# Performance work log

Measured on AMD Instinct MI355X. Metric: run time of the kernel, lower is better.

The kernel has to match this reference:

```python
import jax, jax.numpy as jnp
import numpy as np

TOP_K = 2


def setup_inputs() -> dict:
    key = jax.random.key(0)
    ks = jax.random.split(key, 5)
    B, S, D, F, E = 2, 1024, 1024, 4096, 8
    return {
        "hidden_states": jax.random.normal(ks[0], (B, S, D), jnp.float32),
        "gate_w": jax.random.normal(ks[1], (E, D), jnp.float32) * 0.02,
        "w1": jax.random.normal(ks[2], (E, D, F), jnp.float32) * 0.02,
        "w2": jax.random.normal(ks[3], (E, F, D), jnp.float32) * 0.02,
        "w3": jax.random.normal(ks[4], (E, D, F), jnp.float32) * 0.02,
    }


def reference(hidden_states, gate_w, w1, w2, w3):
    B, S, D = hidden_states.shape
    E = gate_w.shape[0]
    x = hidden_states.reshape(-1, D).astype(jnp.float32)  # [T, D]
    T = x.shape[0]

    # Router: softmax over experts, top-k, renormalize selected weights.
    router_logits = x @ gate_w.T                      # [T, E]
    probs = jax.nn.softmax(router_logits, axis=-1)
    top_w, top_e = jax.lax.top_k(probs, TOP_K)        # [T, K]
    top_w = top_w / jnp.sum(top_w, axis=-1, keepdims=True)

    # Combine weights [T, E]: weight of expert e for token t (0 if not selected).
    combine = jnp.zeros((T, E), jnp.float32).at[jnp.arange(T)[:, None], top_e].add(top_w)

    # Expert SwiGLU FFNs (vectorized over experts; unselected contributions are
    # zeroed by combine weights, matching the gather/scatter math exactly).
    h = jnp.einsum('td,edf->etf', x, w1)              # [E, T, F]
    g = jnp.einsum('td,edf->etf', x, w3)              # [E, T, F]
    y = jnp.einsum('etf,efd->etd', jax.nn.silu(h) * g, w2)  # [E, T, D]

    out = jnp.einsum('etd,te->td', y, combine)        # weighted scatter-combine
    return out.reshape(B, S, D), router_logits
```

## Files before the change

### kernel.cpp

```cpp
#include <hip/hip_runtime.h>
#include <hip/hip_bf16.h>
#include <math.h>

#define T_TOK   2048
#define DDIM    1024
#define FDIM    4096
#define NEXP    8
#define MAXROWS 4608

typedef __bf16          bf16x8 __attribute__((ext_vector_type(8)));
typedef float           f32x4  __attribute__((ext_vector_type(4)));
typedef unsigned short  u16x8  __attribute__((ext_vector_type(8)));

#define LDSP 40
#define FCW  128

static __device__ __forceinline__ unsigned short f2b(float f) {
    __hip_bfloat16 h = __float2bfloat16(f);
    return __builtin_bit_cast(unsigned short, h);
}

static __device__ __forceinline__ void gll16(const unsigned short* g, unsigned short* l) {
    __builtin_amdgcn_global_load_lds(
        (const __attribute__((address_space(1))) unsigned int*)g,
        (__attribute__((address_space(3))) unsigned int*)l, 16, 0, 0);
}

__global__ __launch_bounds__(256) void moe_router_kernel(
    const float* __restrict__ x, const float* __restrict__ gate_w,
    float* __restrict__ logits_out, int* __restrict__ top_e, float* __restrict__ top_w)
{
    int wid  = (blockIdx.x * blockDim.x + threadIdx.x) >> 6;
    int lane = threadIdx.x & 63;
    if (wid >= T_TOK) return;
    const float* xr = x + (size_t)wid * DDIM;
    float acc[NEXP];
    #pragma unroll
    for (int e = 0; e < NEXP; ++e) acc[e] = 0.f;
    for (int d = lane; d < DDIM; d += 64) {
        float xv = xr[d];
        #pragma unroll
        for (int e = 0; e < NEXP; ++e) acc[e] += xv * gate_w[e * DDIM + d];
    }
    #pragma unroll
    for (int e = 0; e < NEXP; ++e) {
        #pragma unroll
        for (int off = 32; off > 0; off >>= 1)
            acc[e] += __shfl_down(acc[e], off, 64);
    }
    if (lane == 0) {
        #pragma unroll
        for (int e = 0; e < NEXP; ++e) logits_out[wid * NEXP + e] = acc[e];
        int e1 = 0;
        #pragma unroll
        for (int e = 1; e < NEXP; ++e) if (acc[e] > acc[e1]) e1 = e;
        int e2 = (e1 == 0) ? 1 : 0;
        #pragma unroll
        for (int e = 0; e < NEXP; ++e) if (e != e1 && acc[e] > acc[e2]) e2 = e;
        float p2 = __expf(acc[e2] - acc[e1]);
        float s  = 1.0f + p2;
        top_e[wid * 2]     = e1;
        top_e[wid * 2 + 1] = e2;
        top_w[wid * 2]     = 1.0f / s;
        top_w[wid * 2 + 1] = p2 / s;
    }
}

__global__ void moe_scatter_kernel(const int* __restrict__ top_e, const float* __restrict__ top_w,
                                   int* __restrict__ cnt, int* __restrict__ list_tok,
                                   float* __restrict__ list_w)
{
    int t = blockIdx.x * blockDim.x + threadIdx.x;
    if (t >= T_TOK) return;
    #pragma unroll
    for (int s = 0; s < 2; ++s) {
        int e   = top_e[t * 2 + s];
        int pos = atomicAdd(&cnt[e], 1);
        list_tok[e * T_TOK + pos] = t;
        list_w [e * T_TOK + pos] = top_w[t * 2 + s];
    }
}

__global__ void moe_prefix_kernel(const int* __restrict__ cnt, int* __restrict__ offs)
{
    if (threadIdx.x == 0 && blockIdx.x == 0) {
        int o = 0;
        #pragma unroll
        for (int e = 0; e < NEXP; ++e) { offs[e] = o; o += ((cnt[e] + 63) >> 6) << 6; }
        offs[NEXP] = o;
    }
}

__global__ __launch_bounds__(256) void transpose_cvt_kernel(
    const float* __restrict__ src, unsigned short* __restrict__ dst, int R, int C)
{
    int tilesC = C >> 6;
    int tilesPerMat = (R >> 6) * tilesC;
    int e  = blockIdx.x / tilesPerMat;
    int t  = blockIdx.x - e * tilesPerMat;
    int tr = t / tilesC, tc = t - tr * tilesC;
    const float*    s = src + (size_t)e * R * C + (size_t)(tr * 64) * C + tc * 64;
    unsigned short* d = dst + (size_t)e * R * C + (size_t)(tc * 64) * R + tr * 64;

    __shared__ unsigned short lds[64][72];
    int tid = threadIdx.x;
    int rr = tid >> 4, cc = (tid & 15) * 4;
    #pragma unroll
    for (int i = 0; i < 4; ++i) {
        int r = rr + 16 * i;
        float4 v = *(const float4*)(s + (size_t)r * C + cc);
        lds[cc + 0][r] = f2b(v.x); lds[cc + 1][r] = f2b(v.y);
        lds[cc + 2][r] = f2b(v.z); lds[cc + 3][r] = f2b(v.w);
    }
    __syncthreads();
    int orow = tid >> 2, oc = (tid & 3) * 16;
    u16x8 a = *(const u16x8*)&lds[orow][oc];
    u16x8 b = *(const u16x8*)&lds[orow][oc + 8];
    *(u16x8*)(d + (size_t)orow * R + oc)     = a;
    *(u16x8*)(d + (size_t)orow * R + oc + 8) = b;
}

__global__ __launch_bounds__(256) void moe_gather_kernel(
    const float* __restrict__ x, const int* __restrict__ list_tok,
    const int* __restrict__ cnt, const int* __restrict__ offs,
    unsigned short* __restrict__ xg)
{
    int e  = blockIdx.x >> 8;
    int rb = blockIdx.x & 255;
    int n = cnt[e];
    int npad = (n + 63) & ~63;
    if (rb * 8 >= npad) return;
    int base = offs[e];
    int tid = threadIdx.x;
    #pragma unroll
    for (int i = 0; i < 4; ++i) {
        int u = tid + 256 * i;
        int r = u >> 7, cu = u & 127;
        int slot = rb * 8 + r;
        int tok = list_tok[e * T_TOK + slot];
        const float* sp = x + (size_t)tok * DDIM + cu * 8;
        float4 v0 = *(const float4*)(sp);
        float4 v1 = *(const float4*)(sp + 4);
        u16x8 t8;
        t8[0]=f2b(v0.x); t8[1]=f2b(v0.y); t8[2]=f2b(v0.z); t8[3]=f2b(v0.w);
        t8[4]=f2b(v1.x); t8[5]=f2b(v1.y); t8[6]=f2b(v1.z); t8[7]=f2b(v1.w);
        *(u16x8*)(xg + (size_t)(base + slot) * DDIM + cu * 8) = t8;
    }
}

__global__ __launch_bounds__(256, 2) void moe_up_kernel(
    const unsigned short* __restrict__ xg,
    const unsigned short* __restrict__ w1t, const unsigned short* __restrict__ w3t,
    const int* __restrict__ cnt, const int* __restrict__ offs,
    unsigned short* __restrict__ act)
{
    const int NWG = NEXP * 32 * 16;
    int logical = (blockIdx.x & 7) * (NWG >> 3) + (blockIdx.x >> 3);
    int mt = logical & 15;
    int fc = (logical >> 4) & 31;
    int e  = logical >> 9;
    int n = cnt[e];
    int npad = (n + 63) & ~63;
    if (mt * 128 >= npad) return;
    int rowBase  = offs[e] + mt * 128;
    int rowMax   = offs[e] + npad - 1;
    int rowLimit = offs[e] + npad;

    __shared__ unsigned short As [128 * 32];
    __shared__ unsigned short B1s[128 * 32];
    __shared__ unsigned short B2s[128 * 32];

    int tid = threadIdx.x;
    int lane = tid & 63, wv = tid >> 6;
    int c = lane & 15, g = lane >> 4;
    int wr = (wv >> 1) * 64, wc = (wv & 1) * 64;

    int srow = tid >> 2, skc = tid & 3;
    int r0 = min(rowBase + srow,      rowMax);
    int r1 = min(rowBase + 64 + srow, rowMax);
    const unsigned short* gA0 = xg + (size_t)r0 * DDIM + skc * 8;
    const unsigned short* gA1 = xg + (size_t)r1 * DDIM + skc * 8;
    size_t wb = (size_t)e * FDIM * DDIM + (size_t)(fc * 128 + srow) * DDIM + skc * 8;
    const unsigned short* gB1a = w1t + wb;
    const unsigned short* gB1b = w1t + wb + (size_t)64 * DDIM;
    const unsigned short* gB2a = w3t + wb;
    const unsigned short* gB2b = w3t + wb + (size_t)64 * DDIM;
    unsigned short* lA0 = As  + tid * 8;
    unsigned short* lA1 = As  + 2048 + tid * 8;
    unsigned short* lB1a = B1s + tid * 8;
    unsigned short* lB1b = B1s + 2048 + tid * 8;
    unsigned short* lB2a = B2s + tid * 8;
    unsigned short* lB2b = B2s + 2048 + tid * 8;

    f32x4 acc_h[4][4], acc_g[4][4];
    #pragma unroll
    for (int i = 0; i < 4; ++i)
        #pragma unroll
        for (int j = 0; j < 4; ++j) { acc_h[i][j] = (f32x4)(0.f); acc_g[i][j] = (f32x4)(0.f); }

    for (int k0 = 0; k0 < DDIM; k0 += 32) {
        gll16(gA0  + k0, lA0);
        gll16(gA1  + k0, lA1);
        gll16(gB1a + k0, lB1a);
        gll16(gB1b + k0, lB1b);
        gll16(gB2a + k0, lB2a);
        gll16(gB2b + k0, lB2b);
        __syncthreads();

        bf16x8 af[4];
        #pragma unroll
        for (int mi = 0; mi < 4; ++mi)
            af[mi] = *reinterpret_cast<const bf16x8*>(&As[(wr + mi * 16 + c) * 32 + g * 8]);
        #pragma unroll
        for (int ni = 0; ni < 4; ++ni) {
            bf16x8 b1 = *reinterpret_cast<const bf16x8*>(&B1s[(wc + ni * 16 + c) * 32 + g * 8]);
            bf16x8 b2 = *reinterpret_cast<const bf16x8*>(&B2s[(wc + ni * 16 + c) * 32 + g * 8]);
            #pragma unroll
            for (int mi = 0; mi < 4; ++mi) {
                acc_h[mi][ni] = __builtin_amdgcn_mfma_f32_16x16x32_bf16(af[mi], b1, acc_h[mi][ni], 0, 0, 0);
                acc_g[mi][ni] = __builtin_amdgcn_mfma_f32_16x16x32_bf16(af[mi], b2, acc_g[mi][ni], 0, 0, 0);
            }
        }
        __syncthreads();
    }

    #pragma unroll
    for (int mi = 0; mi < 4; ++mi) {
        int row = rowBase + wr + mi * 16 + 4 * g;
        if (row < rowLimit) {
            #pragma unroll
            for (int ni = 0; ni < 4; ++ni) {
                int col = fc * 128 + wc + ni * 16 + c;
                #pragma unroll
                for (int r = 0; r < 4; ++r) {
                    float h  = acc_h[mi][ni][r];
                    float gg = acc_g[mi][ni][r];
                    float a  = h / (1.f + __expf(-h)) * gg;
                    act[(size_t)(row + r) * FDIM + col] = f2b(a);
                }
            }
        }
    }
}

__global__ __launch_bounds__(256, 3) void moe_down_kernel(
    const unsigned short* __restrict__ act, const unsigned short* __restrict__ w2t,
    const int* __restrict__ cnt, const int* __restrict__ offs,
    const int* __restrict__ list_tok, const float* __restrict__ list_w,
    float* __restrict__ out)
{
    const int NWG = NEXP * 4 * 8 * 16;
    int logical = (blockIdx.x & 7) * (NWG >> 3) + (blockIdx.x >> 3);
    int mt = logical & 15;
    int dc = (logical >> 4) & 7;
    int ks = (logical >> 7) & 3;
    int e  = logical >> 9;
    int n = cnt[e];
    int npad = (n + 63) & ~63;
    if (mt * 128 >= npad) return;
    int rowBase = offs[e] + mt * 128;
    int rowMax  = offs[e] + npad - 1;

    __shared__ unsigned short As[128 * 32];
    __shared__ unsigned short Bs[128 * 32];

    int tid = threadIdx.x;
    int lane = tid & 63, wv = tid >> 6;
    int c = lane & 15, g = lane >> 4;
    int wr = (wv >> 1) * 64, wc = (wv & 1) * 64;

    int srow = tid >> 2, skc = tid & 3;
    int r0 = min(rowBase + srow,      rowMax);
    int r1 = min(rowBase + 64 + srow, rowMax);
    const unsigned short* gA0 = act + (size_t)r0 * FDIM + ks * 1024 + skc * 8;
    const unsigned short* gA1 = act + (size_t)r1 * FDIM + ks * 1024 + skc * 8;
    size_t wb = (size_t)e * DDIM * FDIM + (size_t)(dc * 128 + srow) * FDIM + ks * 1024 + skc * 8;
    const unsigned short* gBa = w2t + wb;
    const unsigned short* gBb = w2t + wb + (size_t)64 * FDIM;
    unsigned short* lA0 = As + tid * 8;
    unsigned short* lA1 = As + 2048 + tid * 8;
    unsigned short* lBa = Bs + tid * 8;
    unsigned short* lBb = Bs + 2048 + tid * 8;

    f32x4 acc[4][4];
    #pragma unroll
    for (int i = 0; i < 4; ++i)
        #pragma unroll
        for (int j = 0; j < 4; ++j) acc[i][j] = (f32x4)(0.f);

    for (int k0 = 0; k0 < 1024; k0 += 32) {
        gll16(gA0 + k0, lA0);
        gll16(gA1 + k0, lA1);
        gll16(gBa + k0, lBa);
        gll16(gBb + k0, lBb);
        __syncthreads();

        bf16x8 af[4];
        #pragma unroll
        for (int mi = 0; mi < 4; ++mi)
            af[mi] = *reinterpret_cast<const bf16x8*>(&As[(wr + mi * 16 + c) * 32 + g * 8]);
        #pragma unroll
        for (int ni = 0; ni < 4; ++ni) {
            bf16x8 b = *reinterpret_cast<const bf16x8*>(&Bs[(wc + ni * 16 + c) * 32 + g * 8]);
            #pragma unroll
            for (int mi = 0; mi < 4; ++mi)
                acc[mi][ni] = __builtin_amdgcn_mfma_f32_16x16x32_bf16(af[mi], b, acc[mi][ni], 0, 0, 0);
        }
        __syncthreads();
    }

    #pragma unroll
    for (int mi = 0; mi < 4; ++mi) {
        #pragma unroll
        for (int r = 0; r < 4; ++r) {
            int s = mt * 128 + wr + mi * 16 + 4 * g + r;
            if (s < n) {
                int   tok = list_tok[e * T_TOK + s];
                float wt  = list_w [e * T_TOK + s];
                #pragma unroll
                for (int ni = 0; ni < 4; ++ni) {
                    int col = dc * 128 + wc + ni * 16 + c;
                    atomicAdd(&out[(size_t)tok * DDIM + col], wt * acc[mi][ni][r]);
                }
            }
        }
    }
}

__global__ __launch_bounds__(256, 3) void moe_up_legacy(
    const float* __restrict__ x, const float* __restrict__ w1, const float* __restrict__ w3,
    const int* __restrict__ cnt, const int* __restrict__ offs,
    const int* __restrict__ list_tok, unsigned short* __restrict__ act)
{
    const int NWG = NEXP * 32 * 32;
    int bid     = blockIdx.x;
    int logical = (bid & 7) * (NWG >> 3) + (bid >> 3);
    int tile = logical & 31;
    int fc   = (logical >> 5) & 31;
    int e    = logical >> 10;
    int n = cnt[e];
    if (tile * 64 >= n) return;

    __shared__ unsigned short As [64  * LDSP];
    __shared__ unsigned short B1s[FCW * LDSP];
    __shared__ unsigned short B2s[FCW * LDSP];

    int tid = threadIdx.x;
    int lane = tid & 63, wv = tid >> 6;
    int c = lane & 15, g = lane >> 4;
    int ar = tid >> 2, akq = tid & 3;
    int tok = list_tok[e * T_TOK + tile * 64 + ar];
    const float* xrow = x + (size_t)tok * DDIM + akq * 8;
    int bcol = tid & 127, bkh = tid >> 7;
    const size_t wbase = (size_t)e * DDIM * FDIM + (size_t)fc * FCW + bcol;
    const float* w1c = w1 + wbase;
    const float* w3c = w3 + wbase;

    f32x4 acc_h[4][2], acc_g[4][2];
    #pragma unroll
    for (int i = 0; i < 4; ++i)
        #pragma unroll
        for (int j = 0; j < 2; ++j) { acc_h[i][j] = (f32x4)(0.f); acc_g[i][j] = (f32x4)(0.f); }

    for (int k0 = 0; k0 < DDIM; k0 += 32) {
        {
            const float4 v0 = *(const float4*)(xrow + k0);
            const float4 v1 = *(const float4*)(xrow + k0 + 4);
            u16x8 t8;
            t8[0]=f2b(v0.x); t8[1]=f2b(v0.y); t8[2]=f2b(v0.z); t8[3]=f2b(v0.w);
            t8[4]=f2b(v1.x); t8[5]=f2b(v1.y); t8[6]=f2b(v1.z); t8[7]=f2b(v1.w);
            *reinterpret_cast<u16x8*>(&As[ar * LDSP + akq * 8]) = t8;
        }
        {
            int kb = k0 + bkh * 16;
            u16x8 t1a, t1b, t2a, t2b;
            #pragma unroll
            for (int j = 0; j < 8; ++j) {
                t1a[j] = f2b(w1c[(size_t)(kb + j)     * FDIM]);
                t1b[j] = f2b(w1c[(size_t)(kb + 8 + j) * FDIM]);
                t2a[j] = f2b(w3c[(size_t)(kb + j)     * FDIM]);
                t2b[j] = f2b(w3c[(size_t)(kb + 8 + j) * FDIM]);
            }
            *reinterpret_cast<u16x8*>(&B1s[bcol * LDSP + bkh * 16])     = t1a;
            *reinterpret_cast<u16x8*>(&B1s[bcol * LDSP + bkh * 16 + 8]) = t1b;
            *reinterpret_cast<u16x8*>(&B2s[bcol * LDSP + bkh * 16])     = t2a;
            *reinterpret_cast<u16x8*>(&B2s[bcol * LDSP + bkh * 16 + 8]) = t2b;
        }
        __syncthreads();
        bf16x8 af[4];
        #pragma unroll
        for (int mi = 0; mi < 4; ++mi)
            af[mi] = *reinterpret_cast<const bf16x8*>(&As[(mi * 16 + c) * LDSP + g * 8]);
        #pragma unroll
        for (int ni = 0; ni < 2; ++ni) {
            int col = wv * 32 + ni * 16 + c;
            bf16x8 b1 = *reinterpret_cast<const bf16x8*>(&B1s[col * LDSP + g * 8]);
            bf16x8 b2 = *reinterpret_cast<const bf16x8*>(&B2s[col * LDSP + g * 8]);
            #pragma unroll
            for (int mi = 0; mi < 4; ++mi) {
                acc_h[mi][ni] = __builtin_amdgcn_mfma_f32_16x16x32_bf16(af[mi], b1, acc_h[mi][ni], 0, 0, 0);
                acc_g[mi][ni] = __builtin_amdgcn_mfma_f32_16x16x32_bf16(af[mi], b2, acc_g[mi][ni], 0, 0, 0);
            }
        }
        __syncthreads();
    }
    int rowBase = offs[e] + tile * 64;
    #pragma unroll
    for (int mi = 0; mi < 4; ++mi)
        #pragma unroll
        for (int ni = 0; ni < 2; ++ni)
            #pragma unroll
            for (int r = 0; r < 4; ++r) {
                float h  = acc_h[mi][ni][r];
                float gg = acc_g[mi][ni][r];
                float a  = h / (1.f + __expf(-h)) * gg;
                int row = rowBase + mi * 16 + 4 * g + r;
                int col = fc * FCW + wv * 32 + ni * 16 + c;
                act[(size_t)row * FDIM + col] = f2b(a);
            }
}

__global__ __launch_bounds__(256, 4) void moe_down_legacy(
    const unsigned short* __restrict__ act, const float* __restrict__ w2,
    const int* __restrict__ cnt, const int* __restrict__ offs,
    const int* __restrict__ list_tok, const float* __restrict__ list_w,
    float* __restrict__ out)
{
    const int NWG = NEXP * 4 * 4 * 32;
    int bid     = blockIdx.x;
    int logical = (bid & 7) * (NWG >> 3) + (bid >> 3);
    int tile = logical & 31;
    int ks   = (logical >> 5) & 3;
    int dc   = (logical >> 7) & 3;
    int e    = logical >> 9;
    int n = cnt[e];
    if (tile * 64 >= n) return;

    __shared__ unsigned short As[64  * LDSP];
    __shared__ unsigned short Bs[256 * LDSP];
    int tid = threadIdx.x;
    int lane = tid & 63, wv = tid >> 6;
    int c = lane & 15, g = lane >> 4;
    int rowBase = offs[e] + tile * 64;
    int ar = tid >> 2, akq = tid & 3;
    const unsigned short* arow = act + (size_t)(rowBase + ar) * FDIM + ks * 1024 + akq * 8;
    const float* w2c = w2 + (size_t)e * FDIM * DDIM + (size_t)(ks * 1024) * DDIM + (size_t)dc * 256 + tid;

    f32x4 acc[4][4];
    #pragma unroll
    for (int i = 0; i < 4; ++i)
        #pragma unroll
        for (int j = 0; j < 4; ++j) acc[i][j] = (f32x4)(0.f);

    for (int k0 = 0; k0 < 1024; k0 += 32) {
        *reinterpret_cast<u16x8*>(&As[ar * LDSP + akq * 8]) = *reinterpret_cast<const u16x8*>(arow + k0);
        #pragma unroll
        for (int kk = 0; kk < 4; ++kk) {
            u16x8 t1;
            #pragma unroll
            for (int j = 0; j < 8; ++j)
                t1[j] = f2b(w2c[(size_t)(k0 + kk * 8 + j) * DDIM]);
            *reinterpret_cast<u16x8*>(&Bs[tid * LDSP + kk * 8]) = t1;
        }
        __syncthreads();
        bf16x8 af[4];
        #pragma unroll
        for (int mi = 0; mi < 4; ++mi)
            af[mi] = *reinterpret_cast<const bf16x8*>(&As[(mi * 16 + c) * LDSP + g * 8]);
        #pragma unroll
        for (int ni = 0; ni < 4; ++ni) {
            bf16x8 b = *reinterpret_cast<const bf16x8*>(&Bs[(wv * 64 + ni * 16 + c) * LDSP + g * 8]);
            #pragma unroll
            for (int mi = 0; mi < 4; ++mi)
                acc[mi][ni] = __builtin_amdgcn_mfma_f32_16x16x32_bf16(af[mi], b, acc[mi][ni], 0, 0, 0);
        }
        __syncthreads();
    }
    #pragma unroll
    for (int mi = 0; mi < 4; ++mi)
        #pragma unroll
        for (int r = 0; r < 4; ++r) {
            int s = tile * 64 + mi * 16 + 4 * g + r;
            if (s < n) {
                int   tok = list_tok[e * T_TOK + s];
                float wt  = list_w [e * T_TOK + s];
                #pragma unroll
                for (int ni = 0; ni < 4; ++ni) {
                    int col = dc * 256 + wv * 64 + ni * 16 + c;
                    atomicAdd(&out[(size_t)tok * DDIM + col], wt * acc[mi][ni][r]);
                }
            }
        }
}

extern "C" void kernel_launch(void* const* d_in, const int* in_sizes, int n_in,
                              void* d_out, int out_size, void* d_ws, size_t ws_size,
                              hipStream_t stream) {
    const float* x      = (const float*)d_in[0];
    const float* gate_w = (const float*)d_in[1];
    const float* w1     = (const float*)d_in[2];
    const float* w2     = (const float*)d_in[3];
    const float* w3     = (const float*)d_in[4];
    float* out        = (float*)d_out;
    float* logits_out = out + (size_t)T_TOK * DDIM;

    char* ws = (char*)d_ws;
    int*   cnt      = (int*)  (ws);
    int*   offs     = (int*)  (ws + 64);
    int*   top_e    = (int*)  (ws + 1024);
    float* top_w    = (float*)(ws + 17408);
    int*   list_tok = (int*)  (ws + 33792);
    float* list_w   = (float*)(ws + 99328);

    hipMemsetAsync(cnt, 0, 64, stream);
    hipMemsetAsync(list_tok, 0, 131072, stream);
    hipMemsetAsync(out, 0, (size_t)T_TOK * DDIM * sizeof(float), stream);

    moe_router_kernel <<<T_TOK / 4,   256, 0, stream>>>(x, gate_w, logits_out, top_e, top_w);
    moe_scatter_kernel<<<T_TOK / 256, 256, 0, stream>>>(top_e, top_w, cnt, list_tok, list_w);
    moe_prefix_kernel <<<1, 64, 0, stream>>>(cnt, offs);

    const size_t MB = 1u << 20;
    const size_t NEED = 241 * MB;
    if (ws_size >= NEED) {
        unsigned short* xg  = (unsigned short*)(ws + 1   * MB);
        unsigned short* act = (unsigned short*)(ws + 11  * MB);
        unsigned short* w1t = (unsigned short*)(ws + 49  * MB);
        unsigned short* w3t = (unsigned short*)(ws + 113 * MB);
        unsigned short* w2t = (unsigned short*)(ws + 177 * MB);

        moe_gather_kernel<<<NEXP * 256, 256, 0, stream>>>(x, list_tok, cnt, offs, xg);
        transpose_cvt_kernel<<<NEXP * 16 * 64, 256, 0, stream>>>(w1, w1t, DDIM, FDIM);
        transpose_cvt_kernel<<<NEXP * 16 * 64, 256, 0, stream>>>(w3, w3t, DDIM, FDIM);
        transpose_cvt_kernel<<<NEXP * 64 * 16, 256, 0, stream>>>(w2, w2t, FDIM, DDIM);

        moe_up_kernel   <<<NEXP * 32 * 16,    256, 0, stream>>>(xg, w1t, w3t, cnt, offs, act);
        moe_down_kernel <<<NEXP * 4 * 8 * 16, 256, 0, stream>>>(act, w2t, cnt, offs, list_tok, list_w, out);
    } else {
        unsigned short* act = (unsigned short*)(ws + 164864);
        moe_up_legacy   <<<NEXP * 32 * 32,    256, 0, stream>>>(x, w1, w3, cnt, offs, list_tok, act);
        moe_down_legacy <<<NEXP * 4 * 4 * 32, 256, 0, stream>>>(act, w2, cnt, offs, list_tok, list_w, out);
    }
}
```

Before: 416.8 us.

## Fuse w1/w3 transpose, remap MoE block indices, raise GEMM occupancy

Merges the two transpose-convert launches for w1 and w3 into one kernel that handles both matrices per tile, saving a launch and reusing index math. The up and down GEMM kernels get a new block-to-tile mapping: expert in the low bits, then M tile outermost, so early-exit blocks for unused M tiles are spread out and blocks sharing weight columns run close together. Launch bounds rise to 4 waves per SIMD, which may force register spills given the 32 accumulator vectors in the up kernel.

```diff
diff --git a/kernel.cpp b/kernel.cpp
--- a/kernel.cpp
+++ b/kernel.cpp
@@ -88,6 +88,43 @@
         #pragma unroll
         for (int e = 0; e < NEXP; ++e) { offs[e] = o; o += ((cnt[e] + 63) >> 6) << 6; }
         offs[NEXP] = o;
+    }
+}
+
+__global__ __launch_bounds__(256) void transpose_cvt2_kernel(
+    const float* __restrict__ srcA, unsigned short* __restrict__ dstA,
+    const float* __restrict__ srcB, unsigned short* __restrict__ dstB, int R, int C)
+{
+    int tilesC = C >> 6;
+    int tilesPerMat = (R >> 6) * tilesC;
+    int e  = blockIdx.x / tilesPerMat;
+    int t  = blockIdx.x - e * tilesPerMat;
+    int tr = t / tilesC, tc = t - tr * tilesC;
+    size_t soff = (size_t)e * R * C + (size_t)(tr * 64) * C + tc * 64;
+    size_t doff = (size_t)e * R * C + (size_t)(tc * 64) * R + tr * 64;
+
+    __shared__ unsigned short lds[64][72];
+    int tid = threadIdx.x;
+    int rr = tid >> 4, cc = (tid & 15) * 4;
+    int orow = tid >> 2, oc = (tid & 3) * 16;
+
+    #pragma unroll
+    for (int m = 0; m < 2; ++m) {
+        const float*    s = (m == 0 ? srcA : srcB) + soff;
+        unsigned short* d = (m == 0 ? dstA : dstB) + doff;
+        if (m) __syncthreads();
+        #pragma unroll
+        for (int i = 0; i < 4; ++i) {
+            int r = rr + 16 * i;
+            float4 v = *(const float4*)(s + (size_t)r * C + cc);
+            lds[cc + 0][r] = f2b(v.x); lds[cc + 1][r] = f2b(v.y);
+            lds[cc + 2][r] = f2b(v.z); lds[cc + 3][r] = f2b(v.w);
+        }
+        __syncthreads();
+        u16x8 a = *(const u16x8*)&lds[orow][oc];
+        u16x8 b = *(const u16x8*)&lds[orow][oc + 8];
+        *(u16x8*)(d + (size_t)orow * R + oc)     = a;
+        *(u16x8*)(d + (size_t)orow * R + oc + 8) = b;
     }
 }
 
@@ -148,17 +185,16 @@
     }
 }
 
-__global__ __launch_bounds__(256, 2) void moe_up_kernel(
+__global__ __launch_bounds__(256, 4) void moe_up_kernel(
     const unsigned short* __restrict__ xg,
     const unsigned short* __restrict__ w1t, const unsigned short* __restrict__ w3t,
     const int* __restrict__ cnt, const int* __restrict__ offs,
     unsigned short* __restrict__ act)
 {
-    const int NWG = NEXP * 32 * 16;
-    int logical = (blockIdx.x & 7) * (NWG >> 3) + (blockIdx.x >> 3);
-    int mt = logical & 15;
-    int fc = (logical >> 4) & 31;
-    int e  = logical >> 9;
+    int e   = blockIdx.x & 7;
+    int idx = blockIdx.x >> 3;
+    int mt  = idx >> 5;
+    int fc  = idx & 31;
     int n = cnt[e];
     int npad = (n + 63) & ~63;
     if (mt * 128 >= npad) return;
@@ -185,8 +221,8 @@
     const unsigned short* gB1b = w1t + wb + (size_t)64 * DDIM;
     const unsigned short* gB2a = w3t + wb;
     const unsigned short* gB2b = w3t + wb + (size_t)64 * DDIM;
-    unsigned short* lA0 = As  + tid * 8;
-    unsigned short* lA1 = As  + 2048 + tid * 8;
+    unsigned short* lA0  = As  + tid * 8;
+    unsigned short* lA1  = As  + 2048 + tid * 8;
     unsigned short* lB1a = B1s + tid * 8;
     unsigned short* lB1b = B1s + 2048 + tid * 8;
     unsigned short* lB2a = B2s + tid * 8;
@@ -243,18 +279,17 @@
     }
 }
 
-__global__ __launch_bounds__(256, 3) void moe_down_kernel(
+__global__ __launch_bounds__(256, 4) void moe_down_kernel(
     const unsigned short* __restrict__ act, const unsigned short* __restrict__ w2t,
     const int* __restrict__ cnt, const int* __restrict__ offs,
     const int* __restrict__ list_tok, const float* __restrict__ list_w,
     float* __restrict__ out)
 {
-    const int NWG = NEXP * 4 * 8 * 16;
-    int logical = (blockIdx.x & 7) * (NWG >> 3) + (blockIdx.x >> 3);
-    int mt = logical & 15;
-    int dc = (logical >> 4) & 7;
-    int ks = (logical >> 7) & 3;
-    int e  = logical >> 9;
+    int e   = blockIdx.x & 7;
+    int idx = blockIdx.x >> 3;
+    int mt  = idx >> 5;
+    int ks  = (idx >> 3) & 3;
+    int dc  = idx & 7;
     int n = cnt[e];
     int npad = (n + 63) & ~63;
     if (mt * 128 >= npad) return;
@@ -530,12 +565,11 @@
         unsigned short* w2t = (unsigned short*)(ws + 177 * MB);
 
         moe_gather_kernel<<<NEXP * 256, 256, 0, stream>>>(x, list_tok, cnt, offs, xg);
-        transpose_cvt_kernel<<<NEXP * 16 * 64, 256, 0, stream>>>(w1, w1t, DDIM, FDIM);
-        transpose_cvt_kernel<<<NEXP * 16 * 64, 256, 0, stream>>>(w3, w3t, DDIM, FDIM);
-        transpose_cvt_kernel<<<NEXP * 64 * 16, 256, 0, stream>>>(w2, w2t, FDIM, DDIM);
-
-        moe_up_kernel   <<<NEXP * 32 * 16,    256, 0, stream>>>(xg, w1t, w3t, cnt, offs, act);
-        moe_down_kernel <<<NEXP * 4 * 8 * 16, 256, 0, stream>>>(act, w2t, cnt, offs, list_tok, list_w, out);
+        transpose_cvt2_kernel<<<NEXP * 16 * 64, 256, 0, stream>>>(w1, w1t, w3, w3t, DDIM, FDIM);
+        transpose_cvt_kernel <<<NEXP * 64 * 16, 256, 0, stream>>>(w2, w2t, FDIM, DDIM);
+
+        moe_up_kernel   <<<NEXP * 16 * 32, 256, 0, stream>>>(xg, w1t, w3t, cnt, offs, act);
+        moe_down_kernel <<<NEXP * 16 * 32, 256, 0, stream>>>(act, w2t, cnt, offs, list_tok, list_w, out);
     } else {
         unsigned short* act = (unsigned short*)(ws + 164864);
         moe_up_legacy   <<<NEXP * 32 * 32,    256, 0, stream>>>(x, w1, w3, cnt, offs, list_tok, act);
```

New measurement: 1.180 ms. 183% more time.
